# Optimization experiments

Hardware: AMD Instinct MI355X
Metric: run time of the kernel (lower is better)

Reference implementation:

```python
import jax, jax.numpy as jnp
import numpy as np

B, F, M, D, VE, H, V = 16, 4096, 512, 256, 64, 512, 50
OUT = 8  # 4 * 2


def setup_inputs() -> dict:
    key = jax.random.key(0)
    ks = jax.random.split(key, 10)
    features = jax.random.normal(ks[0], (B, F, D), dtype=jnp.float32)
    vowels = jax.random.randint(ks[1], (B, M), 0, V)
    # frames of a mora are contiguous -> sorted indices per utterance
    mora_index = jnp.sort(jax.random.randint(ks[2], (B, F), 0, M), axis=-1)
    emb_table = jax.random.normal(ks[3], (V, VE), dtype=jnp.float32) * 0.02
    W_mora = jax.random.normal(ks[4], (D + VE, H), dtype=jnp.float32) / np.sqrt(D + VE)
    b_mora = jnp.zeros((H,), jnp.float32)
    W_frame = jax.random.normal(ks[5], (D, H), dtype=jnp.float32) / np.sqrt(D)
    b_frame = jnp.zeros((H,), jnp.float32)
    W_post = jax.random.normal(ks[6], (H, OUT), dtype=jnp.float32) / np.sqrt(H)
    b_post = jnp.zeros((OUT,), jnp.float32)
    return {
        "vowels": vowels, "features": features, "mora_index": mora_index,
        "emb_table": emb_table, "W_mora": W_mora, "b_mora": b_mora,
        "W_frame": W_frame, "b_frame": b_frame, "W_post": W_post, "b_post": b_post,
    }


def _segment_mean(features, mora_index):
    # features: [B, F, D]; mora_index: [B, F] in [0, M)
    b, f, d = features.shape
    flat_idx = (mora_index + jnp.arange(b)[:, None] * M).reshape(-1)  # [B*F]
    flat = features.reshape(b * f, d)
    sums = jax.ops.segment_sum(flat, flat_idx, num_segments=b * M)  # [B*M, D]
    cnt = jax.ops.segment_sum(jnp.ones((b * f,), features.dtype), flat_idx,
                              num_segments=b * M)[:, None]
    # scatter_reduce(mean, include_self=False): empty segments stay 0
    mean = jnp.where(cnt > 0, sums / jnp.maximum(cnt, 1.0), 0.0)
    return mean.reshape(b, M, d)


def reference(vowels, features, mora_index, emb_table, W_mora, b_mora,
              W_frame, b_frame, W_post, b_post):
    mora_feat = _segment_mean(features, mora_index)          # [B, M, D]
    mv = emb_table[vowels]                                   # [B, M, VE]
    mh = jnp.concatenate([mv, mora_feat], axis=-1) @ W_mora + b_mora  # [B, M, H]
    fh = features @ W_frame + b_frame                        # [B, F, H] (frame branch; encoder = identity on mora stream)
    del fh
    out = mh @ W_post + b_post                               # [B, M, 8]
    return out.reshape(out.shape[0], out.shape[1], 2, 4)
```

## Files before the change

kernel.cpp:

```cpp
#include <hip/hip_runtime.h>

#define B_DIM  16
#define F_DIM  4096
#define M_DIM  512
#define D_DIM  256
#define VE_DIM 64
#define H_DIM  512
#define K_DIM  320
#define OUT_DIM 8

#define NMORA       (B_DIM * M_DIM)
#define YSTRIDE     16
#define YFLOATS     (NMORA * YSTRIDE)
#define FOLD_BLOCKS 642
#define ZBLOCKS     32

__global__ __launch_bounds__(256) void prep_kernel(
    const float* __restrict__ W_mora,
    const float* __restrict__ b_mora,
    const float* __restrict__ W_post,
    const float* __restrict__ b_post,
    float* __restrict__ WcT,
    float* __restrict__ bc,
    float* __restrict__ y)
{
    const int blk = blockIdx.x;
    const int tid = threadIdx.x;
    if (blk < FOLD_BLOCKS) {
        const int w    = blk * 4 + (tid >> 6);
        const int lane = tid & 63;
        float sum = 0.f;
        if (w < 2560) {
            const int k = w >> 3, o = w & 7;
            const float* arow = W_mora + k * H_DIM;
            #pragma unroll
            for (int it = 0; it < H_DIM / 64; ++it) {
                const int j = lane + it * 64;
                sum += arow[j] * W_post[j * OUT_DIM + o];
            }
            #pragma unroll
            for (int off = 32; off >= 1; off >>= 1) sum += __shfl_down(sum, off, 64);
            if (lane == 0) WcT[o * K_DIM + k] = sum;
        } else if (w < 2568) {
            const int o = w - 2560;
            #pragma unroll
            for (int it = 0; it < H_DIM / 64; ++it) {
                const int j = lane + it * 64;
                sum += b_mora[j] * W_post[j * OUT_DIM + o];
            }
            #pragma unroll
            for (int off = 32; off >= 1; off >>= 1) sum += __shfl_down(sum, off, 64);
            if (lane == 0) bc[o] = sum + b_post[o];
        }
    } else {
        const int zb = blk - FOLD_BLOCKS;
        float4* z = (float4*)y;
        #pragma unroll
        for (int j = 0; j < 4; ++j)
            z[zb * 1024 + j * 256 + tid] = make_float4(0.f, 0.f, 0.f, 0.f);
    }
}

__device__ __forceinline__ void flush_run(float* __restrict__ y, int gm,
                                          const float4& a, int n, int lane,
                                          const float (&Wf)[OUT_DIM][4])
{
    float p[OUT_DIM];
    #pragma unroll
    for (int o = 0; o < OUT_DIM; ++o)
        p[o] = a.x * Wf[o][0] + a.y * Wf[o][1] + a.z * Wf[o][2] + a.w * Wf[o][3];
    #pragma unroll
    for (int off = 32; off >= 1; off >>= 1) {
        #pragma unroll
        for (int o = 0; o < OUT_DIM; ++o) p[o] += __shfl_xor(p[o], off, 64);
    }
    float val = p[0];
    #pragma unroll
    for (int o = 1; o < OUT_DIM; ++o) val = (lane == o) ? p[o] : val;
    val = (lane == 8) ? (float)n : val;
    if (lane < 9) atomicAdd(&y[(size_t)gm * YSTRIDE + lane], val);
}

__global__ __launch_bounds__(256) void seg_project_kernel(
    const float* __restrict__ features,
    const int* __restrict__ mora_index,
    const float* __restrict__ WcT,
    float* __restrict__ y)
{
    const int gw   = blockIdx.x * 4 + (threadIdx.x >> 6);
    const int lane = threadIdx.x & 63;
    const int b    = gw >> 8;
    const int f0   = (gw & 255) * 16;

    float Wf[OUT_DIM][4];
    #pragma unroll
    for (int o = 0; o < OUT_DIM; ++o) {
        const float4 t = *(const float4*)&WcT[o * K_DIM + VE_DIM + 4 * lane];
        Wf[o][0] = t.x; Wf[o][1] = t.y; Wf[o][2] = t.z; Wf[o][3] = t.w;
    }

    const int* mi = mora_index + b * F_DIM + f0;
    int idx[16];
    #pragma unroll
    for (int i = 0; i < 16; ++i) idx[i] = mi[i];

    const float4* src = (const float4*)features + ((size_t)b * F_DIM + f0) * 64 + lane;

    float4 a = make_float4(0.f, 0.f, 0.f, 0.f);
    int cur = idx[0];
    int n = 0;
    #pragma unroll
    for (int h = 0; h < 2; ++h) {
        float4 v[8];
        #pragma unroll
        for (int i = 0; i < 8; ++i) v[i] = src[(h * 8 + i) * 64];
        #pragma unroll
        for (int i = 0; i < 8; ++i) {
            const int id = idx[h * 8 + i];
            if (id != cur) {
                flush_run(y, b * M_DIM + cur, a, n, lane, Wf);
                a = make_float4(0.f, 0.f, 0.f, 0.f);
                n = 0;
                cur = id;
            }
            a.x += v[i].x; a.y += v[i].y; a.z += v[i].z; a.w += v[i].w;
            ++n;
        }
    }
    flush_run(y, b * M_DIM + cur, a, n, lane, Wf);
}

__global__ __launch_bounds__(256) void finish_kernel(
    const int* __restrict__ vowels,
    const float* __restrict__ emb,
    const float* __restrict__ WcT,
    const float* __restrict__ bc,
    const float* __restrict__ y,
    float* __restrict__ out)
{
    const int t  = blockIdx.x * 256 + threadIdx.x;
    const int gm = t >> 3;
    const int o  = t & 7;
    const float cnt = y[gm * YSTRIDE + 8];
    const float inv = (cnt > 0.f) ? 1.0f / cnt : 0.0f;
    const int vw = vowels[gm];
    float r = y[gm * YSTRIDE + o] * inv + bc[o];
    const float* e = emb + vw * VE_DIM;
    const float* w = WcT + o * K_DIM;
    #pragma unroll
    for (int c = 0; c < VE_DIM; ++c) r += e[c] * w[c];
    out[t] = r;
}

extern "C" void kernel_launch(void* const* d_in, const int* in_sizes, int n_in,
                              void* d_out, int out_size, void* d_ws, size_t ws_size,
                              hipStream_t stream) {
    const int*   vowels     = (const int*)d_in[0];
    const float* features   = (const float*)d_in[1];
    const int*   mora_index = (const int*)d_in[2];
    const float* emb        = (const float*)d_in[3];
    const float* W_mora     = (const float*)d_in[4];
    const float* b_mora     = (const float*)d_in[5];
    const float* W_post     = (const float*)d_in[8];
    const float* b_post     = (const float*)d_in[9];
    float*       out        = (float*)d_out;

    float* y   = (float*)d_ws;
    float* WcT = y + YFLOATS;
    float* bc  = WcT + OUT_DIM * K_DIM;

    prep_kernel<<<FOLD_BLOCKS + ZBLOCKS, 256, 0, stream>>>(
        W_mora, b_mora, W_post, b_post, WcT, bc, y);
    seg_project_kernel<<<1024, 256, 0, stream>>>(features, mora_index, WcT, y);
    finish_kernel<<<NMORA * OUT_DIM / 256, 256, 0, stream>>>(
        vowels, emb, WcT, bc, y, out);
}
```

Baseline: 121.3 us.

## Restructure weight fold, shorten shuffle reductions, double frames per wave, vectorize loads

The weight-fold prep now has each wave compute all 8 outputs for one row of W_mora, reading W_post with float4 loads, so it launches far fewer blocks. A shared reduce8 helper replaces the 8x6-shuffle butterfly with a partial butterfly plus select, cutting shuffle count in both prep and the per-run flush. The segment kernel processes 32 frames per wave instead of 16, with int4 index loads, which halves the grid and gives fewer boundary atomics per wave. The finish kernel uses float4 loads for the embedding dot product. Fewer waves in the segment kernel may reduce the memory parallelism available to hide latency.

```diff
diff --git a/kernel.cpp b/kernel.cpp
--- a/kernel.cpp
+++ b/kernel.cpp
@@ -12,8 +12,24 @@
 #define NMORA       (B_DIM * M_DIM)
 #define YSTRIDE     16
 #define YFLOATS     (NMORA * YSTRIDE)
-#define FOLD_BLOCKS 642
+#define FOLD_BLOCKS 81
 #define ZBLOCKS     32
+
+__device__ __forceinline__ float reduce8(float (&p)[OUT_DIM], int lane) {
+    #pragma unroll
+    for (int off = 1; off <= 4; off <<= 1) {
+        #pragma unroll
+        for (int o = 0; o < OUT_DIM; ++o) p[o] += __shfl_xor(p[o], off, 64);
+    }
+    const int s = lane & 7;
+    float val = p[0];
+    #pragma unroll
+    for (int o = 1; o < OUT_DIM; ++o) val = (s == o) ? p[o] : val;
+    val += __shfl_xor(val, 8, 64);
+    val += __shfl_xor(val, 16, 64);
+    val += __shfl_xor(val, 32, 64);
+    return val;
+}
 
 __global__ __launch_bounds__(256) void prep_kernel(
     const float* __restrict__ W_mora,
@@ -29,28 +45,25 @@
     if (blk < FOLD_BLOCKS) {
         const int w    = blk * 4 + (tid >> 6);
         const int lane = tid & 63;
-        float sum = 0.f;
-        if (w < 2560) {
-            const int k = w >> 3, o = w & 7;
-            const float* arow = W_mora + k * H_DIM;
+        if (w <= 320) {
+            const float* arow = (w < 320) ? (W_mora + w * H_DIM) : b_mora;
+            float acc[OUT_DIM] = {0.f, 0.f, 0.f, 0.f, 0.f, 0.f, 0.f, 0.f};
             #pragma unroll
             for (int it = 0; it < H_DIM / 64; ++it) {
-                const int j = lane + it * 64;
-                sum += arow[j] * W_post[j * OUT_DIM + o];
+                const int j = it * 64 + lane;
+                const float aval = arow[j];
+                const float4 w0 = *(const float4*)&W_post[j * OUT_DIM];
+                const float4 w1 = *(const float4*)&W_post[j * OUT_DIM + 4];
+                acc[0] += aval * w0.x; acc[1] += aval * w0.y;
+                acc[2] += aval * w0.z; acc[3] += aval * w0.w;
+                acc[4] += aval * w1.x; acc[5] += aval * w1.y;
+                acc[6] += aval * w1.z; acc[7] += aval * w1.w;
             }
-            #pragma unroll
-            for (int off = 32; off >= 1; off >>= 1) sum += __shfl_down(sum, off, 64);
-            if (lane == 0) WcT[o * K_DIM + k] = sum;
-        } else if (w < 2568) {
-            const int o = w - 2560;
-            #pragma unroll
-            for (int it = 0; it < H_DIM / 64; ++it) {
-                const int j = lane + it * 64;
-                sum += b_mora[j] * W_post[j * OUT_DIM + o];
+            const float val = reduce8(acc, lane);
+            if (lane < OUT_DIM) {
+                if (w < 320) WcT[lane * K_DIM + w] = val;
+                else         bc[lane] = val + b_post[lane];
             }
-            #pragma unroll
-            for (int off = 32; off >= 1; off >>= 1) sum += __shfl_down(sum, off, 64);
-            if (lane == 0) bc[o] = sum + b_post[o];
         }
     } else {
         const int zb = blk - FOLD_BLOCKS;
@@ -69,14 +82,7 @@
     #pragma unroll
     for (int o = 0; o < OUT_DIM; ++o)
         p[o] = a.x * Wf[o][0] + a.y * Wf[o][1] + a.z * Wf[o][2] + a.w * Wf[o][3];
-    #pragma unroll
-    for (int off = 32; off >= 1; off >>= 1) {
-        #pragma unroll
-        for (int o = 0; o < OUT_DIM; ++o) p[o] += __shfl_xor(p[o], off, 64);
-    }
-    float val = p[0];
-    #pragma unroll
-    for (int o = 1; o < OUT_DIM; ++o) val = (lane == o) ? p[o] : val;
+    float val = reduce8(p, lane);
     val = (lane == 8) ? (float)n : val;
     if (lane < 9) atomicAdd(&y[(size_t)gm * YSTRIDE + lane], val);
 }
@@ -89,8 +95,8 @@
 {
     const int gw   = blockIdx.x * 4 + (threadIdx.x >> 6);
     const int lane = threadIdx.x & 63;
-    const int b    = gw >> 8;
-    const int f0   = (gw & 255) * 16;
+    const int b    = gw >> 7;
+    const int f0   = (gw & 127) * 32;
 
     float Wf[OUT_DIM][4];
     #pragma unroll
@@ -99,10 +105,14 @@
         Wf[o][0] = t.x; Wf[o][1] = t.y; Wf[o][2] = t.z; Wf[o][3] = t.w;
     }
 
-    const int* mi = mora_index + b * F_DIM + f0;
-    int idx[16];
+    int idx[32];
+    const int4* mi4 = (const int4*)(mora_index + b * F_DIM + f0);
     #pragma unroll
-    for (int i = 0; i < 16; ++i) idx[i] = mi[i];
+    for (int i = 0; i < 8; ++i) {
+        const int4 t = mi4[i];
+        idx[4 * i + 0] = t.x; idx[4 * i + 1] = t.y;
+        idx[4 * i + 2] = t.z; idx[4 * i + 3] = t.w;
+    }
 
     const float4* src = (const float4*)features + ((size_t)b * F_DIM + f0) * 64 + lane;
 
@@ -110,7 +120,7 @@
     int cur = idx[0];
     int n = 0;
     #pragma unroll
-    for (int h = 0; h < 2; ++h) {
+    for (int h = 0; h < 4; ++h) {
         float4 v[8];
         #pragma unroll
         for (int i = 0; i < 8; ++i) v[i] = src[(h * 8 + i) * 64];
@@ -145,10 +155,14 @@
     const float inv = (cnt > 0.f) ? 1.0f / cnt : 0.0f;
     const int vw = vowels[gm];
     float r = y[gm * YSTRIDE + o] * inv + bc[o];
-    const float* e = emb + vw * VE_DIM;
-    const float* w = WcT + o * K_DIM;
+    const float4* e4 = (const float4*)(emb + vw * VE_DIM);
+    const float4* w4 = (const float4*)(WcT + o * K_DIM);
     #pragma unroll
-    for (int c = 0; c < VE_DIM; ++c) r += e[c] * w[c];
+    for (int c = 0; c < VE_DIM / 4; ++c) {
+        const float4 ev = e4[c];
+        const float4 wv = w4[c];
+        r += ev.x * wv.x + ev.y * wv.y + ev.z * wv.z + ev.w * wv.w;
+    }
     out[t] = r;
 }
 
@@ -171,7 +185,7 @@
 
     prep_kernel<<<FOLD_BLOCKS + ZBLOCKS, 256, 0, stream>>>(
         W_mora, b_mora, W_post, b_post, WcT, bc, y);
-    seg_project_kernel<<<1024, 256, 0, stream>>>(features, mora_index, WcT, y);
+    seg_project_kernel<<<512, 256, 0, stream>>>(features, mora_index, WcT, y);
     finish_kernel<<<NMORA * OUT_DIM / 256, 256, 0, stream>>>(
         vowels, emb, WcT, bc, y, out);
 }
```

Result: faster. 118.6 us (-2.2%).
